# Kernel tuning notes

Hardware: AMD Instinct MI355X
Metric: run time of the kernel (lower is better)

The kernel has to match this reference:

```python
import jax, jax.numpy as jnp
import numpy as np

B, L, N, H = 4, 8192, 16, 64
BASE = 10000.0
N_SEG = 16  # packed segments per row, each of length L // N_SEG


def setup_inputs() -> dict:
    key = jax.random.key(0)
    x = jax.random.normal(key, (B, L, N, H), dtype=jnp.float32)
    # index_tensor: lengths of packed sub-sequences at the front of each row,
    # zeros elsewhere (matches the module's docstring convention). Sum == L.
    seg_len = L // N_SEG
    idx = np.zeros((B, L), dtype=np.int64)
    idx[:, :N_SEG] = seg_len
    return {"x": x, "index_tensor": jnp.asarray(idx)}


def _positions(index_tensor, L):
    """Segment-reset positions: concat of arange(l) for each length l, zero-padded.

    Zero-length entries contribute empty aranges, so filtering nonzeros (as the
    torch code does) is equivalent to cumulative-sum bookkeeping over raw lengths.
    """
    def row(lengths):
        csum = jnp.cumsum(lengths)          # inclusive cumsum of segment lengths
        starts = csum - lengths             # exclusive cumsum = segment start offsets
        j = jnp.arange(L)
        seg = jnp.clip(jnp.searchsorted(csum, j, side='right'), 0, L - 1)
        return jnp.where(j < csum[-1], j - starts[seg], 0)
    return jax.vmap(row)(index_tensor).astype(jnp.float32)  # [B, L]


def reference(x, index_tensor):
    Bx, Lx, n, h = x.shape
    inv_freq = 1.0 / BASE ** (jnp.arange(0, h, 2, dtype=jnp.float32) / h)  # [h/2]
    pos = _positions(index_tensor, Lx)                    # [B, L]
    freqs = pos[..., None] * inv_freq                     # [B, L, h/2]
    emb = jnp.concatenate([freqs, freqs], axis=-1)        # [B, L, h]
    cos = jnp.cos(emb)[:, :, None, :]                     # [B, L, 1, h]
    sin = jnp.sin(emb)[:, :, None, :]
    x1, x2 = jnp.split(x, 2, axis=-1)
    rot = jnp.concatenate([-x2, x1], axis=-1)             # rotate_half
    return x * cos + rot * sin
```

## Files before the change

### kernel.cpp

```cpp
#include <hip/hip_runtime.h>
#include <cmath>

#define B_ 4
#define L_ 8192
#define N_ 16
#define H_ 64

typedef float f32x4 __attribute__((ext_vector_type(4)));

__global__ __launch_bounds__(1024)
void pos_kernel(const long long* __restrict__ idx, float* __restrict__ pos) {
    __shared__ int csum[L_];
    __shared__ int wp[17];
    const int b   = blockIdx.x;
    const int tid = threadIdx.x;
    constexpr int CHUNK = L_ / 1024;

    const long long* row = idx + (size_t)b * L_;

    int local[CHUNK];
    int s = 0;
#pragma unroll
    for (int i = 0; i < CHUNK; ++i) {
        s += (int)row[tid * CHUNK + i];
        local[i] = s;
    }

    const int lane = tid & 63, wv = tid >> 6;
    int scan = s;
#pragma unroll
    for (int off = 1; off < 64; off <<= 1) {
        int n = __shfl_up(scan, off);
        if (lane >= off) scan += n;
    }
    if (lane == 63) wp[wv + 1] = scan;
    if (tid == 0)   wp[0] = 0;
    __syncthreads();
    if (tid == 0) {
        int a = 0;
        for (int i = 1; i <= 16; ++i) { a += wp[i]; wp[i] = a; }
    }
    __syncthreads();

    const int off0 = wp[wv] + (scan - s);
#pragma unroll
    for (int i = 0; i < CHUNK; ++i) csum[tid * CHUNK + i] = off0 + local[i];
    __syncthreads();

    const int total = csum[L_ - 1];

    int p[CHUNK];
#pragma unroll
    for (int u = 0; u < CHUNK; ++u) p[u] = 0;
#pragma unroll
    for (int k = L_ / 2; k > 0; k >>= 1) {
#pragma unroll
        for (int u = 0; u < CHUNK; ++u) {
            const int j = tid + u * 1024;
            p[u] += (csum[p[u] + k - 1] <= j) ? k : 0;
        }
    }
#pragma unroll
    for (int u = 0; u < CHUNK; ++u) {
        const int j    = tid + u * 1024;
        const int excl = p[u] ? csum[p[u] - 1] : 0;
        pos[(size_t)b * L_ + j] = (j < total) ? (float)(j - excl) : 0.f;
    }
}

__global__ void rope_kernel(const float* __restrict__ x,
                            const float* __restrict__ pos,
                            float* __restrict__ out) {
    const size_t t  = (size_t)blockIdx.x * blockDim.x + threadIdx.x;
    const int    q  = (int)(t & 7);
    const int    hh = (int)((t >> 3) & 1);
    const size_t bl = t >> 4;

    const float p = pos[bl];

    constexpr float NEG_LN_BASE_OVER_32 = -0.28782313662425f;
    constexpr float INV_2PI             = 0.15915493667126f;

    float sv[4], cv[4];
#pragma unroll
    for (int j = 0; j < 4; ++j) {
        const float f  = __expf((float)(q * 4 + j) * NEG_LN_BASE_OVER_32);
        float ph = p * f * INV_2PI;
        ph -= floorf(ph);
        sv[j] = __builtin_amdgcn_sinf(ph);
        cv[j] = __builtin_amdgcn_cosf(ph);
    }

    const size_t base0 = (bl * N_ + (size_t)(hh * 8)) * H_ + (size_t)(q * 4);
#pragma unroll
    for (int n = 0; n < 8; ++n) {
        const size_t base = base0 + (size_t)n * H_;
        const f32x4 a = __builtin_nontemporal_load((const f32x4*)(x + base));
        const f32x4 b = __builtin_nontemporal_load((const f32x4*)(x + base + 32));
        f32x4 o1, o2;
#pragma unroll
        for (int j = 0; j < 4; ++j) {
            const float xa = a[j];
            const float xb = b[j];
            o1[j] = xa * cv[j] - xb * sv[j];
            o2[j] = xb * cv[j] + xa * sv[j];
        }
        __builtin_nontemporal_store(o1, (f32x4*)(out + base));
        __builtin_nontemporal_store(o2, (f32x4*)(out + base + 32));
    }
}

extern "C" void kernel_launch(void* const* d_in, const int* in_sizes, int n_in,
                              void* d_out, int out_size, void* d_ws, size_t ws_size,
                              hipStream_t stream) {
    const float*     x   = (const float*)d_in[0];
    const long long* idx = (const long long*)d_in[1];
    float*           out = (float*)d_out;
    float*           pos = (float*)d_ws;

    pos_kernel<<<B_, 1024, 0, stream>>>(idx, pos);

    const size_t total_threads = (size_t)B_ * L_ * 16;
    const int    blocks        = (int)(total_threads / 256);
    rope_kernel<<<blocks, 256, 0, stream>>>(x, pos, out);
}
```

Before: 55.54 us.

## Restructure RoPE kernel as coalesced grid-stride loop with lane-shuffle rotate_half

Rewrites the rope kernel so each thread handles one contiguous float4 per iteration over a fixed 2048-block grid. The rotate_half partner is obtained with a cross-lane xor shuffle instead of a second strided load. Frequencies are precomputed per thread, but sin/cos are now recomputed per element rather than reused across 8 heads. The aim is fully coalesced access and fewer blocks, at the cost of more transcendental ALU work.

```diff
diff --git a/kernel.cpp b/kernel.cpp
--- a/kernel.cpp
+++ b/kernel.cpp
@@ -68,45 +68,47 @@
     }
 }
 
-__global__ void rope_kernel(const float* __restrict__ x,
-                            const float* __restrict__ pos,
-                            float* __restrict__ out) {
-    const size_t t  = (size_t)blockIdx.x * blockDim.x + threadIdx.x;
-    const int    q  = (int)(t & 7);
-    const int    hh = (int)((t >> 3) & 1);
-    const size_t bl = t >> 4;
+__global__ __launch_bounds__(256)
+void rope_kernel(const float* __restrict__ x,
+                 const float* __restrict__ pos,
+                 float* __restrict__ out) {
+    constexpr int NTHR  = 524288;
+    constexpr int ITERS = (B_ * L_ * N_ * H_ / 4) / NTHR;
 
-    const float p = pos[bl];
+    const int t  = blockIdx.x * 256 + threadIdx.x;
+    const int qp = t & 15;
+    const float sgn = (qp < 8) ? -1.f : 1.f;
 
     constexpr float NEG_LN_BASE_OVER_32 = -0.28782313662425f;
     constexpr float INV_2PI             = 0.15915493667126f;
+    float f[4];
+#pragma unroll
+    for (int j = 0; j < 4; ++j)
+        f[j] = __expf((float)((qp & 7) * 4 + j) * NEG_LN_BASE_OVER_32) * INV_2PI;
 
-    float sv[4], cv[4];
+#pragma unroll 4
+    for (int i = 0; i < ITERS; ++i) {
+        const size_t v  = (size_t)t + (size_t)i * NTHR;
+        const size_t bl = v >> 8;
+        const float  p  = pos[bl];
+
+        const f32x4 a = __builtin_nontemporal_load((const f32x4*)(x) + v);
+
+        f32x4 pr;
 #pragma unroll
-    for (int j = 0; j < 4; ++j) {
-        const float f  = __expf((float)(q * 4 + j) * NEG_LN_BASE_OVER_32);
-        float ph = p * f * INV_2PI;
-        ph -= floorf(ph);
-        sv[j] = __builtin_amdgcn_sinf(ph);
-        cv[j] = __builtin_amdgcn_cosf(ph);
-    }
+        for (int j = 0; j < 4; ++j) pr[j] = __shfl_xor(a[j], 8);
 
-    const size_t base0 = (bl * N_ + (size_t)(hh * 8)) * H_ + (size_t)(q * 4);
-#pragma unroll
-    for (int n = 0; n < 8; ++n) {
-        const size_t base = base0 + (size_t)n * H_;
-        const f32x4 a = __builtin_nontemporal_load((const f32x4*)(x + base));
-        const f32x4 b = __builtin_nontemporal_load((const f32x4*)(x + base + 32));
-        f32x4 o1, o2;
+        f32x4 o;
 #pragma unroll
         for (int j = 0; j < 4; ++j) {
-            const float xa = a[j];
-            const float xb = b[j];
-            o1[j] = xa * cv[j] - xb * sv[j];
-            o2[j] = xb * cv[j] + xa * sv[j];
+            float ph = p * f[j];
+            ph -= floorf(ph);
+            const float cv = __builtin_amdgcn_cosf(ph);
+            const float sv = __builtin_amdgcn_sinf(ph);
+            o[j] = a[j] * cv + sgn * pr[j] * sv;
         }
-        __builtin_nontemporal_store(o1, (f32x4*)(out + base));
-        __builtin_nontemporal_store(o2, (f32x4*)(out + base + 32));
+
+        __builtin_nontemporal_store(o, (f32x4*)(out) + v);
     }
 }
 
@@ -119,8 +121,5 @@
     float*           pos = (float*)d_ws;
 
     pos_kernel<<<B_, 1024, 0, stream>>>(idx, pos);
-
-    const size_t total_threads = (size_t)B_ * L_ * 16;
-    const int    blocks        = (int)(total_threads / 256);
-    rope_kernel<<<blocks, 256, 0, stream>>>(x, pos, out);
+    rope_kernel<<<2048, 256, 0, stream>>>(x, pos, out);
 }
```

Measured after the change: 60.33 us. +8.6%, slower.
